# Kernel optimization log

Hardware: AMD Instinct MI355X
Metric: run time of the kernel (lower is better)

The kernel has to match this reference:

```python
import jax, jax.numpy as jnp
import numpy as np

B, C, H, W = 8, 192, 128, 128
FILTERS = (1, 3, 3, 3, 1)  # 1 -> 3 -> 3 -> 3 -> 1 per-channel MLP
INIT_SCALE = 10.0
BOUND = 1e-9


@jax.custom_vjp
def lower_bound(x):
    return jnp.maximum(x, BOUND)

def _lb_fwd(x):
    return jnp.maximum(x, BOUND), x

def _lb_bwd(x, g):
    # gradient passes when x >= bound OR incoming grad pushes x down further is blocked
    passthrough = (x >= BOUND) | (g < 0)
    return (jnp.where(passthrough, g, jnp.zeros_like(g)),)

lower_bound.defvjp(_lb_fwd, _lb_bwd)


def setup_inputs() -> dict:
    key = jax.random.key(0)
    ks = jax.random.split(key, 20)
    inp = {"x": 2.0 * jax.random.normal(ks[0], (B, C, H, W), jnp.float32)}
    scale = INIT_SCALE ** (1.0 / (len(FILTERS) - 1))
    k = 1
    for i in range(4):
        fin, fout = FILTERS[i], FILTERS[i + 1]
        init = float(np.log(np.expm1(1.0 / scale / fout)))
        inp[f"matrix{i}"] = (jnp.full((C, fout, fin), init, jnp.float32)
                              + 0.02 * jax.random.normal(ks[k], (C, fout, fin), jnp.float32)); k += 1
        inp[f"bias{i}"] = jax.random.uniform(ks[k], (C, fout, 1), jnp.float32, -0.5, 0.5); k += 1
        if i < 3:
            inp[f"factor{i}"] = 0.1 * jax.random.normal(ks[k], (C, fout, 1), jnp.float32); k += 1
    inp["quantiles"] = jnp.broadcast_to(
        jnp.array([-INIT_SCALE, 0.0, INIT_SCALE], jnp.float32), (C, 1, 3)).copy()
    return inp


def _logits_cumulative(v, mats, biases, factors):
    logits = v  # [C, 1, N]
    for i in range(4):
        logits = jnp.einsum('coi,cin->con', jax.nn.softplus(mats[i]), logits) + biases[i]
        if i < 3:
            logits = logits + jnp.tanh(factors[i]) * jnp.tanh(logits)
    return logits  # [C, 1, N]


def reference(x, matrix0, bias0, factor0, matrix1, bias1, factor1,
              matrix2, bias2, factor2, matrix3, bias3, quantiles):
    mats = [matrix0, matrix1, matrix2, matrix3]
    biases = [bias0, bias1, bias2, bias3]
    factors = [factor0, factor1, factor2]
    # channel-first flatten: [B,C,H,W] -> [C, 1, B*H*W]
    x_perm = jnp.transpose(x, (1, 0, 2, 3))
    values = x_perm.reshape(C, 1, -1)
    medians = jax.lax.stop_gradient(quantiles[:, :, 1:2])  # [C,1,1]
    # eval-mode quantize ('dequantize'): round around per-channel median
    outputs = jnp.round(values - medians) + medians
    lower = _logits_cumulative(outputs - 0.5, mats, biases, factors)
    upper = _logits_cumulative(outputs + 0.5, mats, biases, factors)
    sign = jax.lax.stop_gradient(-jnp.sign(lower + upper))
    likelihood = jnp.abs(jax.nn.sigmoid(sign * upper) - jax.nn.sigmoid(sign * lower))
    likelihood = lower_bound(likelihood)
    shape = (C, B, H, W)
    out = jnp.transpose(outputs.reshape(shape), (1, 0, 2, 3))
    lik = jnp.transpose(likelihood.reshape(shape), (1, 0, 2, 3))
    return out, lik
```

## Files before the change

### kernel.cpp

```cpp
#include <hip/hip_runtime.h>
#include <math.h>


constexpr int Bn = 8, Cn = 192, Hn = 128, Wn = 128;
constexpr int HWn = Hn * Wn;
constexpr long long NELEM = (long long)Bn * Cn * HWn;
constexpr int LUTN = 256;
constexpr float BOUND = 1e-9f;

struct Params {
  float med;
  float w0[3], b0[3], f0[3];
  float w1[9], b1[3], f1[3];
  float w2[9], b2[3], f2[3];
  float w3[3], b3;
};


__device__ __forceinline__ float fast_rcp(float x) { return __builtin_amdgcn_rcpf(x); }

__device__ __forceinline__ float fast_tanhx(float x) {
  float e = __expf(2.0f * x);
  return 1.0f - 2.0f * fast_rcp(e + 1.0f);
}
__device__ __forceinline__ float fast_sigmoid(float x) {
  return fast_rcp(1.0f + __expf(-x));
}
__device__ __forceinline__ float acc_sigmoid(float x) {
  return 1.0f / (1.0f + expf(-x));
}
__device__ __forceinline__ float softplus_acc(float x) {
  return fmaxf(x, 0.0f) + log1pf(expf(-fabsf(x)));
}

template <bool ACC>
__device__ __forceinline__ float tanh_sel(float x) {
  return ACC ? tanhf(x) : fast_tanhx(x);
}
template <bool ACC>
__device__ __forceinline__ float sig_sel(float x) {
  return ACC ? acc_sigmoid(x) : fast_sigmoid(x);
}


__device__ __forceinline__ void load_params(
    Params& P, int c,
    const float* __restrict__ m0, const float* __restrict__ b0, const float* __restrict__ f0,
    const float* __restrict__ m1, const float* __restrict__ b1, const float* __restrict__ f1,
    const float* __restrict__ m2, const float* __restrict__ b2, const float* __restrict__ f2,
    const float* __restrict__ m3, const float* __restrict__ b3, const float* __restrict__ q) {
  P.med = q[c * 3 + 1];
#pragma unroll
  for (int j = 0; j < 3; ++j) {
    P.w0[j] = softplus_acc(m0[c * 3 + j]);
    P.b0[j] = b0[c * 3 + j];
    P.f0[j] = tanhf(f0[c * 3 + j]);
    P.b1[j] = b1[c * 3 + j];
    P.f1[j] = tanhf(f1[c * 3 + j]);
    P.b2[j] = b2[c * 3 + j];
    P.f2[j] = tanhf(f2[c * 3 + j]);
    P.w3[j] = softplus_acc(m3[c * 3 + j]);
  }
#pragma unroll
  for (int k = 0; k < 9; ++k) {
    P.w1[k] = softplus_acc(m1[c * 9 + k]);
    P.w2[k] = softplus_acc(m2[c * 9 + k]);
  }
  P.b3 = b3[c];
}


template <bool ACC>
__device__ __forceinline__ float mlp_eval(const Params& P, float t) {
  float h0 = fmaf(P.w0[0], t, P.b0[0]);
  float h1 = fmaf(P.w0[1], t, P.b0[1]);
  float h2 = fmaf(P.w0[2], t, P.b0[2]);
  h0 = fmaf(P.f0[0], tanh_sel<ACC>(h0), h0);
  h1 = fmaf(P.f0[1], tanh_sel<ACC>(h1), h1);
  h2 = fmaf(P.f0[2], tanh_sel<ACC>(h2), h2);

  float g0 = fmaf(P.w1[0], h0, fmaf(P.w1[1], h1, fmaf(P.w1[2], h2, P.b1[0])));
  float g1 = fmaf(P.w1[3], h0, fmaf(P.w1[4], h1, fmaf(P.w1[5], h2, P.b1[1])));
  float g2 = fmaf(P.w1[6], h0, fmaf(P.w1[7], h1, fmaf(P.w1[8], h2, P.b1[2])));
  g0 = fmaf(P.f1[0], tanh_sel<ACC>(g0), g0);
  g1 = fmaf(P.f1[1], tanh_sel<ACC>(g1), g1);
  g2 = fmaf(P.f1[2], tanh_sel<ACC>(g2), g2);

  float q0 = fmaf(P.w2[0], g0, fmaf(P.w2[1], g1, fmaf(P.w2[2], g2, P.b2[0])));
  float q1 = fmaf(P.w2[3], g0, fmaf(P.w2[4], g1, fmaf(P.w2[5], g2, P.b2[1])));
  float q2 = fmaf(P.w2[6], g0, fmaf(P.w2[7], g1, fmaf(P.w2[8], g2, P.b2[2])));
  q0 = fmaf(P.f2[0], tanh_sel<ACC>(q0), q0);
  q1 = fmaf(P.f2[1], tanh_sel<ACC>(q1), q1);
  q2 = fmaf(P.f2[2], tanh_sel<ACC>(q2), q2);

  return fmaf(P.w3[0], q0, fmaf(P.w3[1], q1, fmaf(P.w3[2], q2, P.b3)));
}

template <bool ACC>
__device__ __forceinline__ float likelihood_of(const Params& P, float o) {
  float lo = mlp_eval<ACC>(P, o - 0.5f);
  float up = mlp_eval<ACC>(P, o + 0.5f);
  float su = lo + up;
  float s = (su > 0.0f) ? -1.0f : ((su < 0.0f) ? 1.0f : 0.0f);
  float d = fabsf(sig_sel<ACC>(s * up) - sig_sel<ACC>(s * lo));
  return fmaxf(d, BOUND);
}


__global__ __launch_bounds__(LUTN) void build_lut(
    const float* __restrict__ m0, const float* __restrict__ b0, const float* __restrict__ f0,
    const float* __restrict__ m1, const float* __restrict__ b1, const float* __restrict__ f1,
    const float* __restrict__ m2, const float* __restrict__ b2, const float* __restrict__ f2,
    const float* __restrict__ m3, const float* __restrict__ b3, const float* __restrict__ q,
    float* __restrict__ lut) {
  __shared__ Params P;
  const int c = blockIdx.x;
  if (threadIdx.x == 0) {
    load_params(P, c, m0, b0, f0, m1, b1, f1, m2, b2, f2, m3, b3, q);
  }
  __syncthreads();
  const int t = threadIdx.x;
  const float o = (float)(t - 128) + P.med;
  lut[c * LUTN + t] = likelihood_of<true>(P, o);
}


__global__ __launch_bounds__(256, 8) void eb_lut_main(
    const float* __restrict__ x, const float* __restrict__ q,
    const float* __restrict__ lut, float* __restrict__ out, float* __restrict__ lik) {
  __shared__ float slut[LUTN];
  const int slab = blockIdx.x;
  const int c = slab % Cn;
  slut[threadIdx.x] = lut[c * LUTN + threadIdx.x];
  const float med = q[c * 3 + 1];
  __syncthreads();

  const long long base = (long long)slab * HWn;
  const float4* __restrict__ xin = (const float4*)(x + base);
  float4* __restrict__ po = (float4*)(out + base);
  float4* __restrict__ pl = (float4*)(lik + base);

#pragma unroll
  for (int it = 0; it < HWn / 4 / 256; ++it) {
    const int i = threadIdx.x + it * 256;
    float4 xv = xin[i];
    float4 ov, lv;
    {
      float r = rintf(xv.x - med); ov.x = r + med;
      int idx = (int)r + 128; idx = idx < 0 ? 0 : (idx > 255 ? 255 : idx);
      lv.x = slut[idx];
    }
    {
      float r = rintf(xv.y - med); ov.y = r + med;
      int idx = (int)r + 128; idx = idx < 0 ? 0 : (idx > 255 ? 255 : idx);
      lv.y = slut[idx];
    }
    {
      float r = rintf(xv.z - med); ov.z = r + med;
      int idx = (int)r + 128; idx = idx < 0 ? 0 : (idx > 255 ? 255 : idx);
      lv.z = slut[idx];
    }
    {
      float r = rintf(xv.w - med); ov.w = r + med;
      int idx = (int)r + 128; idx = idx < 0 ? 0 : (idx > 255 ? 255 : idx);
      lv.w = slut[idx];
    }
    po[i] = ov;
    pl[i] = lv;
  }
}


__global__ __launch_bounds__(256, 4) void eb_direct(
    const float* __restrict__ x,
    const float* __restrict__ m0, const float* __restrict__ b0, const float* __restrict__ f0,
    const float* __restrict__ m1, const float* __restrict__ b1, const float* __restrict__ f1,
    const float* __restrict__ m2, const float* __restrict__ b2, const float* __restrict__ f2,
    const float* __restrict__ m3, const float* __restrict__ b3, const float* __restrict__ q,
    float* __restrict__ out, float* __restrict__ lik) {
  __shared__ Params SP;
  const int slab = blockIdx.x;
  const int c = slab % Cn;
  if (threadIdx.x == 0) {
    load_params(SP, c, m0, b0, f0, m1, b1, f1, m2, b2, f2, m3, b3, q);
  }
  __syncthreads();
  Params P = SP;

  const long long base = (long long)slab * HWn;
  const float4* __restrict__ xin = (const float4*)(x + base);
  float4* __restrict__ po = (float4*)(out + base);
  float4* __restrict__ pl = (float4*)(lik + base);

  for (int it = 0; it < HWn / 4 / 256; ++it) {
    const int i = threadIdx.x + it * 256;
    float4 xv = xin[i];
    float4 ov, lv;
    {
      float r = rintf(xv.x - P.med); ov.x = r + P.med; lv.x = likelihood_of<false>(P, ov.x);
    }
    {
      float r = rintf(xv.y - P.med); ov.y = r + P.med; lv.y = likelihood_of<false>(P, ov.y);
    }
    {
      float r = rintf(xv.z - P.med); ov.z = r + P.med; lv.z = likelihood_of<false>(P, ov.z);
    }
    {
      float r = rintf(xv.w - P.med); ov.w = r + P.med; lv.w = likelihood_of<false>(P, ov.w);
    }
    po[i] = ov;
    pl[i] = lv;
  }
}


extern "C" void kernel_launch(void* const* d_in, const int* in_sizes, int n_in,
                              void* d_out, int out_size, void* d_ws, size_t ws_size,
                              hipStream_t stream) {
  const float* x  = (const float*)d_in[0];
  const float* m0 = (const float*)d_in[1];
  const float* b0 = (const float*)d_in[2];
  const float* f0 = (const float*)d_in[3];
  const float* m1 = (const float*)d_in[4];
  const float* b1 = (const float*)d_in[5];
  const float* f1 = (const float*)d_in[6];
  const float* m2 = (const float*)d_in[7];
  const float* b2 = (const float*)d_in[8];
  const float* f2 = (const float*)d_in[9];
  const float* m3 = (const float*)d_in[10];
  const float* b3 = (const float*)d_in[11];
  const float* q  = (const float*)d_in[12];

  float* out = (float*)d_out;
  float* lik = out + NELEM;

  const size_t lut_bytes = (size_t)Cn * LUTN * sizeof(float);
  if (ws_size >= lut_bytes) {
    float* lut = (float*)d_ws;
    build_lut<<<Cn, LUTN, 0, stream>>>(m0, b0, f0, m1, b1, f1, m2, b2, f2, m3, b3, q, lut);
    eb_lut_main<<<Bn * Cn, 256, 0, stream>>>(x, q, lut, out, lik);
  } else {
    eb_direct<<<Bn * Cn, 256, 0, stream>>>(x, m0, b0, f0, m1, b1, f1, m2, b2, f2,
                                           m3, b3, q, out, lik);
  }
}
```

Measured before the change: 310.5 us.

## Fuse per-channel LUT build into main kernel with parallel param load and nontemporal IO

Removes the separate LUT-building kernel and workspace round trip. Each block now computes its own channel's 256-entry likelihood table in shared memory, after loading the parameters in parallel across threads. The streaming loop uses nontemporal loads and stores. This saves a kernel launch and a dependency on global memory. In exchange, the LUT math is repeated once per batch item (8x redundant) at the start of each block, which adds latency before streaming begins.

```diff
diff --git a/kernel.cpp b/kernel.cpp
--- a/kernel.cpp
+++ b/kernel.cpp
@@ -8,6 +8,8 @@
 constexpr int LUTN = 256;
 constexpr float BOUND = 1e-9f;
 
+typedef float f4 __attribute__((ext_vector_type(4)));
+
 struct Params {
   float med;
   float w0[3], b0[3], f0[3];
@@ -16,203 +18,98 @@
   float w3[3], b3;
 };
 
-
-__device__ __forceinline__ float fast_rcp(float x) { return __builtin_amdgcn_rcpf(x); }
-
-__device__ __forceinline__ float fast_tanhx(float x) {
-  float e = __expf(2.0f * x);
-  return 1.0f - 2.0f * fast_rcp(e + 1.0f);
-}
-__device__ __forceinline__ float fast_sigmoid(float x) {
-  return fast_rcp(1.0f + __expf(-x));
-}
-__device__ __forceinline__ float acc_sigmoid(float x) {
-  return 1.0f / (1.0f + expf(-x));
-}
 __device__ __forceinline__ float softplus_acc(float x) {
   return fmaxf(x, 0.0f) + log1pf(expf(-fabsf(x)));
 }
 
-template <bool ACC>
-__device__ __forceinline__ float tanh_sel(float x) {
-  return ACC ? tanhf(x) : fast_tanhx(x);
-}
-template <bool ACC>
-__device__ __forceinline__ float sig_sel(float x) {
-  return ACC ? acc_sigmoid(x) : fast_sigmoid(x);
-}
-
-
-__device__ __forceinline__ void load_params(
-    Params& P, int c,
-    const float* __restrict__ m0, const float* __restrict__ b0, const float* __restrict__ f0,
-    const float* __restrict__ m1, const float* __restrict__ b1, const float* __restrict__ f1,
-    const float* __restrict__ m2, const float* __restrict__ b2, const float* __restrict__ f2,
-    const float* __restrict__ m3, const float* __restrict__ b3, const float* __restrict__ q) {
-  P.med = q[c * 3 + 1];
-#pragma unroll
-  for (int j = 0; j < 3; ++j) {
-    P.w0[j] = softplus_acc(m0[c * 3 + j]);
-    P.b0[j] = b0[c * 3 + j];
-    P.f0[j] = tanhf(f0[c * 3 + j]);
-    P.b1[j] = b1[c * 3 + j];
-    P.f1[j] = tanhf(f1[c * 3 + j]);
-    P.b2[j] = b2[c * 3 + j];
-    P.f2[j] = tanhf(f2[c * 3 + j]);
-    P.w3[j] = softplus_acc(m3[c * 3 + j]);
-  }
-#pragma unroll
-  for (int k = 0; k < 9; ++k) {
-    P.w1[k] = softplus_acc(m1[c * 9 + k]);
-    P.w2[k] = softplus_acc(m2[c * 9 + k]);
-  }
-  P.b3 = b3[c];
-}
-
-
-template <bool ACC>
-__device__ __forceinline__ float mlp_eval(const Params& P, float t) {
+__device__ __forceinline__ float mlp_acc(const Params& P, float t) {
   float h0 = fmaf(P.w0[0], t, P.b0[0]);
   float h1 = fmaf(P.w0[1], t, P.b0[1]);
   float h2 = fmaf(P.w0[2], t, P.b0[2]);
-  h0 = fmaf(P.f0[0], tanh_sel<ACC>(h0), h0);
-  h1 = fmaf(P.f0[1], tanh_sel<ACC>(h1), h1);
-  h2 = fmaf(P.f0[2], tanh_sel<ACC>(h2), h2);
+  h0 = fmaf(P.f0[0], tanhf(h0), h0);
+  h1 = fmaf(P.f0[1], tanhf(h1), h1);
+  h2 = fmaf(P.f0[2], tanhf(h2), h2);
 
   float g0 = fmaf(P.w1[0], h0, fmaf(P.w1[1], h1, fmaf(P.w1[2], h2, P.b1[0])));
   float g1 = fmaf(P.w1[3], h0, fmaf(P.w1[4], h1, fmaf(P.w1[5], h2, P.b1[1])));
   float g2 = fmaf(P.w1[6], h0, fmaf(P.w1[7], h1, fmaf(P.w1[8], h2, P.b1[2])));
-  g0 = fmaf(P.f1[0], tanh_sel<ACC>(g0), g0);
-  g1 = fmaf(P.f1[1], tanh_sel<ACC>(g1), g1);
-  g2 = fmaf(P.f1[2], tanh_sel<ACC>(g2), g2);
+  g0 = fmaf(P.f1[0], tanhf(g0), g0);
+  g1 = fmaf(P.f1[1], tanhf(g1), g1);
+  g2 = fmaf(P.f1[2], tanhf(g2), g2);
 
   float q0 = fmaf(P.w2[0], g0, fmaf(P.w2[1], g1, fmaf(P.w2[2], g2, P.b2[0])));
   float q1 = fmaf(P.w2[3], g0, fmaf(P.w2[4], g1, fmaf(P.w2[5], g2, P.b2[1])));
   float q2 = fmaf(P.w2[6], g0, fmaf(P.w2[7], g1, fmaf(P.w2[8], g2, P.b2[2])));
-  q0 = fmaf(P.f2[0], tanh_sel<ACC>(q0), q0);
-  q1 = fmaf(P.f2[1], tanh_sel<ACC>(q1), q1);
-  q2 = fmaf(P.f2[2], tanh_sel<ACC>(q2), q2);
+  q0 = fmaf(P.f2[0], tanhf(q0), q0);
+  q1 = fmaf(P.f2[1], tanhf(q1), q1);
+  q2 = fmaf(P.f2[2], tanhf(q2), q2);
 
   return fmaf(P.w3[0], q0, fmaf(P.w3[1], q1, fmaf(P.w3[2], q2, P.b3)));
 }
 
-template <bool ACC>
-__device__ __forceinline__ float likelihood_of(const Params& P, float o) {
-  float lo = mlp_eval<ACC>(P, o - 0.5f);
-  float up = mlp_eval<ACC>(P, o + 0.5f);
-  float su = lo + up;
-  float s = (su > 0.0f) ? -1.0f : ((su < 0.0f) ? 1.0f : 0.0f);
-  float d = fabsf(sig_sel<ACC>(s * up) - sig_sel<ACC>(s * lo));
-  return fmaxf(d, BOUND);
-}
-
-
-__global__ __launch_bounds__(LUTN) void build_lut(
-    const float* __restrict__ m0, const float* __restrict__ b0, const float* __restrict__ f0,
-    const float* __restrict__ m1, const float* __restrict__ b1, const float* __restrict__ f1,
-    const float* __restrict__ m2, const float* __restrict__ b2, const float* __restrict__ f2,
-    const float* __restrict__ m3, const float* __restrict__ b3, const float* __restrict__ q,
-    float* __restrict__ lut) {
-  __shared__ Params P;
-  const int c = blockIdx.x;
-  if (threadIdx.x == 0) {
-    load_params(P, c, m0, b0, f0, m1, b1, f1, m2, b2, f2, m3, b3, q);
-  }
-  __syncthreads();
-  const int t = threadIdx.x;
-  const float o = (float)(t - 128) + P.med;
-  lut[c * LUTN + t] = likelihood_of<true>(P, o);
-}
-
-
-__global__ __launch_bounds__(256, 8) void eb_lut_main(
-    const float* __restrict__ x, const float* __restrict__ q,
-    const float* __restrict__ lut, float* __restrict__ out, float* __restrict__ lik) {
-  __shared__ float slut[LUTN];
-  const int slab = blockIdx.x;
-  const int c = slab % Cn;
-  slut[threadIdx.x] = lut[c * LUTN + threadIdx.x];
-  const float med = q[c * 3 + 1];
-  __syncthreads();
-
-  const long long base = (long long)slab * HWn;
-  const float4* __restrict__ xin = (const float4*)(x + base);
-  float4* __restrict__ po = (float4*)(out + base);
-  float4* __restrict__ pl = (float4*)(lik + base);
-
-#pragma unroll
-  for (int it = 0; it < HWn / 4 / 256; ++it) {
-    const int i = threadIdx.x + it * 256;
-    float4 xv = xin[i];
-    float4 ov, lv;
-    {
-      float r = rintf(xv.x - med); ov.x = r + med;
-      int idx = (int)r + 128; idx = idx < 0 ? 0 : (idx > 255 ? 255 : idx);
-      lv.x = slut[idx];
-    }
-    {
-      float r = rintf(xv.y - med); ov.y = r + med;
-      int idx = (int)r + 128; idx = idx < 0 ? 0 : (idx > 255 ? 255 : idx);
-      lv.y = slut[idx];
-    }
-    {
-      float r = rintf(xv.z - med); ov.z = r + med;
-      int idx = (int)r + 128; idx = idx < 0 ? 0 : (idx > 255 ? 255 : idx);
-      lv.z = slut[idx];
-    }
-    {
-      float r = rintf(xv.w - med); ov.w = r + med;
-      int idx = (int)r + 128; idx = idx < 0 ? 0 : (idx > 255 ? 255 : idx);
-      lv.w = slut[idx];
-    }
-    po[i] = ov;
-    pl[i] = lv;
-  }
-}
-
-
-__global__ __launch_bounds__(256, 4) void eb_direct(
+__global__ __launch_bounds__(256, 8) void eb_fused(
     const float* __restrict__ x,
     const float* __restrict__ m0, const float* __restrict__ b0, const float* __restrict__ f0,
     const float* __restrict__ m1, const float* __restrict__ b1, const float* __restrict__ f1,
     const float* __restrict__ m2, const float* __restrict__ b2, const float* __restrict__ f2,
     const float* __restrict__ m3, const float* __restrict__ b3, const float* __restrict__ q,
     float* __restrict__ out, float* __restrict__ lik) {
-  __shared__ Params SP;
+  __shared__ Params P;
+  __shared__ float slut[LUTN];
+
   const int slab = blockIdx.x;
   const int c = slab % Cn;
-  if (threadIdx.x == 0) {
-    load_params(SP, c, m0, b0, f0, m1, b1, f1, m2, b2, f2, m3, b3, q);
+  const int t = threadIdx.x;
+
+  if (t < 3)        P.w0[t]      = softplus_acc(m0[c * 3 + t]);
+  else if (t < 12)  P.w1[t - 3]  = softplus_acc(m1[c * 9 + (t - 3)]);
+  else if (t < 21)  P.w2[t - 12] = softplus_acc(m2[c * 9 + (t - 12)]);
+  else if (t < 24)  P.w3[t - 21] = softplus_acc(m3[c * 3 + (t - 21)]);
+  else if (t < 27)  P.f0[t - 24] = tanhf(f0[c * 3 + (t - 24)]);
+  else if (t < 30)  P.f1[t - 27] = tanhf(f1[c * 3 + (t - 27)]);
+  else if (t < 33)  P.f2[t - 30] = tanhf(f2[c * 3 + (t - 30)]);
+  else if (t < 36)  P.b0[t - 33] = b0[c * 3 + (t - 33)];
+  else if (t < 39)  P.b1[t - 36] = b1[c * 3 + (t - 36)];
+  else if (t < 42)  P.b2[t - 39] = b2[c * 3 + (t - 39)];
+  else if (t == 42) P.b3 = b3[c];
+  else if (t == 43) P.med = q[c * 3 + 1];
+  __syncthreads();
+
+  const float med = P.med;
+
+  {
+    const float o = (float)(t - 128) + med;
+    float lo = mlp_acc(P, o - 0.5f);
+    float up = mlp_acc(P, o + 0.5f);
+    float su = lo + up;
+    float s = (su > 0.0f) ? -1.0f : ((su < 0.0f) ? 1.0f : 0.0f);
+    float d = fabsf(1.0f / (1.0f + expf(-s * up)) - 1.0f / (1.0f + expf(-s * lo)));
+    slut[t] = fmaxf(d, BOUND);
   }
   __syncthreads();
-  Params P = SP;
 
   const long long base = (long long)slab * HWn;
-  const float4* __restrict__ xin = (const float4*)(x + base);
-  float4* __restrict__ po = (float4*)(out + base);
-  float4* __restrict__ pl = (float4*)(lik + base);
+  const f4* __restrict__ xin = (const f4*)(x + base);
+  f4* __restrict__ po = (f4*)(out + base);
+  f4* __restrict__ pl = (f4*)(lik + base);
 
+#pragma unroll
   for (int it = 0; it < HWn / 4 / 256; ++it) {
-    const int i = threadIdx.x + it * 256;
-    float4 xv = xin[i];
-    float4 ov, lv;
-    {
-      float r = rintf(xv.x - P.med); ov.x = r + P.med; lv.x = likelihood_of<false>(P, ov.x);
+    const int i = t + it * 256;
+    f4 xv = __builtin_nontemporal_load(&xin[i]);
+    f4 ov, lv;
+#pragma unroll
+    for (int j = 0; j < 4; ++j) {
+      float r = rintf(xv[j] - med);
+      ov[j] = r + med;
+      int idx = (int)r + 128;
+      idx = idx < 0 ? 0 : (idx > 255 ? 255 : idx);
+      lv[j] = slut[idx];
     }
-    {
-      float r = rintf(xv.y - P.med); ov.y = r + P.med; lv.y = likelihood_of<false>(P, ov.y);
-    }
-    {
-      float r = rintf(xv.z - P.med); ov.z = r + P.med; lv.z = likelihood_of<false>(P, ov.z);
-    }
-    {
-      float r = rintf(xv.w - P.med); ov.w = r + P.med; lv.w = likelihood_of<false>(P, ov.w);
-    }
-    po[i] = ov;
-    pl[i] = lv;
+    __builtin_nontemporal_store(ov, &po[i]);
+    __builtin_nontemporal_store(lv, &pl[i]);
   }
 }
-
 
 extern "C" void kernel_launch(void* const* d_in, const int* in_sizes, int n_in,
                               void* d_out, int out_size, void* d_ws, size_t ws_size,
@@ -234,13 +131,6 @@
   float* out = (float*)d_out;
   float* lik = out + NELEM;
 
-  const size_t lut_bytes = (size_t)Cn * LUTN * sizeof(float);
-  if (ws_size >= lut_bytes) {
-    float* lut = (float*)d_ws;
-    build_lut<<<Cn, LUTN, 0, stream>>>(m0, b0, f0, m1, b1, f1, m2, b2, f2, m3, b3, q, lut);
-    eb_lut_main<<<Bn * Cn, 256, 0, stream>>>(x, q, lut, out, lik);
-  } else {
-    eb_direct<<<Bn * Cn, 256, 0, stream>>>(x, m0, b0, f0, m1, b1, f1, m2, b2, f2,
-                                           m3, b3, q, out, lik);
-  }
+  eb_fused<<<Bn * Cn, 256, 0, stream>>>(x, m0, b0, f0, m1, b1, f1, m2, b2, f2,
+                                        m3, b3, q, out, lik);
 }
```

Measured after the change: 294.0 us. 1.06x faster.
